# Performance work log

Measured on AMD Instinct MI355X. Metric: run time of the kernel, lower is better.

## Reference

```python
import jax, jax.numpy as jnp
import numpy as np

N_NODES = 50000
N_EDGES = 1600000
IN_CH = 256
LAT = 32
HID = 64
OUT_CH = 256
GAT_H = 32  # GAT hidden dims [32, 32], heads=1


def setup_inputs() -> dict:
    key = jax.random.key(0)
    ks = jax.random.split(key, 30)
    nrm = lambda k, shape, s=0.05: jax.random.normal(k, shape, dtype=jnp.float32) * s
    inp = {}
    inp["x"] = jax.random.normal(ks[0], (N_NODES, IN_CH), dtype=jnp.float32)
    inp["edge_index"] = jax.random.randint(ks[1], (2, N_EDGES), 0, N_NODES)
    # GAT layer 1: IN_CH -> 32 (heads=1), layer 2: 32 -> 32, final linear 32 -> LAT
    inp["W_g1"] = nrm(ks[2], (IN_CH, GAT_H)); inp["as_g1"] = nrm(ks[3], (GAT_H,)); inp["ad_g1"] = nrm(ks[4], (GAT_H,)); inp["b_g1"] = jnp.zeros((GAT_H,), jnp.float32)
    inp["W_g2"] = nrm(ks[5], (GAT_H, GAT_H)); inp["as_g2"] = nrm(ks[6], (GAT_H,)); inp["ad_g2"] = nrm(ks[7], (GAT_H,)); inp["b_g2"] = jnp.zeros((GAT_H,), jnp.float32)
    inp["W_gf"] = nrm(ks[8], (GAT_H, LAT)); inp["b_gf"] = jnp.zeros((LAT,), jnp.float32)
    inp["W_m1"] = nrm(ks[9], (IN_CH, HID)); inp["b_m1"] = jnp.zeros((HID,), jnp.float32); inp["g_m1"] = jnp.ones((HID,), jnp.float32); inp["be_m1"] = jnp.zeros((HID,), jnp.float32)
    inp["W_m2"] = nrm(ks[10], (HID, HID)); inp["b_m2"] = jnp.zeros((HID,), jnp.float32); inp["g_m2"] = jnp.ones((HID,), jnp.float32); inp["be_m2"] = jnp.zeros((HID,), jnp.float32)
    inp["W_m3"] = nrm(ks[11], (HID, LAT)); inp["b_m3"] = jnp.zeros((LAT,), jnp.float32); inp["g_m3"] = jnp.ones((LAT,), jnp.float32); inp["be_m3"] = jnp.zeros((LAT,), jnp.float32)
    # final linear LAT -> OUT_CH + ReLU
    inp["W_f"] = nrm(ks[12], (LAT, OUT_CH)); inp["b_f"] = jnp.zeros((OUT_CH,), jnp.float32)
    return inp


def _bn_relu(h, g, b):
    # BatchNorm1d in training mode: batch stats, biased variance, eps=1e-5
    m = jnp.mean(h, axis=0)
    v = jnp.var(h, axis=0)
    return jax.nn.relu((h - m) * jax.lax.rsqrt(v + 1e-5) * g + b)


def _gat(h_in, src, dst, W, a_s, a_d, b):
    # PyG GATConv (heads=1): edge (src j -> dst i), e = LeakyReLU(a_src.Wx_j + a_dst.Wx_i)
    N = h_in.shape[0]
    h = h_in @ W                                   # [N, F]
    e = jax.nn.leaky_relu((h @ a_s)[src] + (h @ a_d)[dst], 0.2)  # [E]
    m = jax.ops.segment_max(e, dst, num_segments=N)              # scatter-softmax over incoming edges
    ex = jnp.exp(e - m[dst])
    den = jax.ops.segment_sum(ex, dst, num_segments=N)
    alpha = ex / den[dst]
    out = jax.ops.segment_sum(alpha[:, None] * h[src], dst, num_segments=N)
    return out + b


def reference(x, edge_index, W_g1, as_g1, ad_g1, b_g1, W_g2, as_g2, ad_g2, b_g2, W_gf, b_gf, W_m1, b_m1, g_m1, be_m1, W_m2, b_m2, g_m2, be_m2, W_m3, b_m3, g_m3, be_m3, W_f, b_f):
    N = x.shape[0]
    loops = jnp.arange(N)
    src = jnp.concatenate([edge_index[0], loops])  # PyG add_self_loops=True
    dst = jnp.concatenate([edge_index[1], loops])
    r = _bn_relu(x @ W_m1 + b_m1, g_m1, be_m1)
    r = _bn_relu(r @ W_m2 + b_m2, g_m2, be_m2)
    r = _bn_relu(r @ W_m3 + b_m3, g_m3, be_m3)
    # GAT interpolation branch (dropout inactive in eval)
    h = jax.nn.relu(_gat(x, src, dst, W_g1, as_g1, ad_g1, b_g1))
    h = jax.nn.relu(_gat(h, src, dst, W_g2, as_g2, ad_g2, b_g2))
    h = h @ W_gf + b_gf
    # blend with alphas = 0.5 constant vector
    out = 0.5 * r + 0.5 * h
    return jax.nn.relu(out @ W_f + b_f)
```

## Files before the change

### kernel.cpp

```cpp
#include <hip/hip_runtime.h>

#define NNODES 50000
#define NEDGES 1600000
#define NBUCK 196
#define BIN_CH 4096
#define CNT_CH 4096

typedef __attribute__((ext_vector_type(4))) float f32x4;
typedef __attribute__((ext_vector_type(8))) short short8;

__device__ __forceinline__ float leaky02(float x) { return x > 0.f ? x : 0.2f * x; }

__device__ __forceinline__ int block_incl_scan(int v, int* sh) {
  int t = threadIdx.x;
  sh[t] = v;
  __syncthreads();
  for (int d = 1; d < 256; d <<= 1) {
    int u = (t >= d) ? sh[t - d] : 0;
    __syncthreads();
    sh[t] += u;
    __syncthreads();
  }
  return sh[t];
}

__global__ __launch_bounds__(256) void k_b0(const int* __restrict__ dst,
                                            int* __restrict__ gcnt, int E) {
  __shared__ int hist[256];
  int t = threadIdx.x;
  hist[t] = 0;
  __syncthreads();
  int base0 = blockIdx.x * CNT_CH;
#pragma unroll
  for (int r = 0; r < CNT_CH / 256; ++r) {
    int idx = base0 + r * 256 + t;
    if (idx < E) atomicAdd(&hist[dst[idx] >> 8], 1);
  }
  __syncthreads();
  if (t < NBUCK && hist[t]) atomicAdd(&gcnt[t], hist[t]);
}

__global__ __launch_bounds__(256) void k_b1(const int* __restrict__ gcnt,
                                            int* __restrict__ base,
                                            int* __restrict__ cursor) {
  __shared__ int sh[256];
  int t = threadIdx.x;
  int v = (t < NBUCK) ? gcnt[t] : 0;
  int incl = block_incl_scan(v, sh);
  if (t < NBUCK) {
    base[t] = incl - v;
    cursor[t] = incl - v;
  }
  if (t == 255) base[NBUCK] = NEDGES;
}

__global__ __launch_bounds__(256) void k_bin(const int* __restrict__ src,
                                             const int* __restrict__ dst,
                                             int* __restrict__ cursor,
                                             unsigned* __restrict__ binned, int E) {
  __shared__ int hist[256];
  __shared__ int cur[256];
  int t = threadIdx.x;
  int base0 = blockIdx.x * BIN_CH;
  unsigned pk[BIN_CH / 256];
  hist[t] = 0;
  __syncthreads();
#pragma unroll
  for (int r = 0; r < BIN_CH / 256; ++r) {
    int idx = base0 + r * 256 + t;
    if (idx < E) {
      unsigned p = ((unsigned)dst[idx] << 16) | (unsigned)src[idx];
      pk[r] = p;
      atomicAdd(&hist[p >> 24], 1);
    }
  }
  __syncthreads();
  if (t < NBUCK && hist[t]) cur[t] = atomicAdd(&cursor[t], hist[t]);
  __syncthreads();
#pragma unroll
  for (int r = 0; r < BIN_CH / 256; ++r) {
    int idx = base0 + r * 256 + t;
    if (idx < E) {
      unsigned p = pk[r];
      int pos = atomicAdd(&cur[p >> 24], 1);
      binned[pos] = p;
    }
  }
}

__global__ __launch_bounds__(256) void k_sort(const unsigned* __restrict__ binned,
                                              const int* __restrict__ base,
                                              int* __restrict__ deg,
                                              int* __restrict__ offs,
                                              int* __restrict__ csr) {
  __shared__ int hist[256];
  __shared__ int scanbuf[256];
  __shared__ int cur[256];
  int t = threadIdx.x;
  int b = blockIdx.x;
  int lo = base[b], hi = base[b + 1];
  int node0 = b << 8;
  hist[t] = 0;
  __syncthreads();
  for (int i = lo + t; i < hi; i += 256)
    atomicAdd(&hist[(binned[i] >> 16) & 255], 1);
  __syncthreads();
  int h = hist[t];
  int incl = block_incl_scan(h, scanbuf);
  int excl = incl - h;
  int node = node0 + t;
  if (node < NNODES) {
    deg[node] = h;
    offs[node] = lo + excl;
  }
  cur[t] = lo + excl;
  __syncthreads();
  for (int i = lo + t; i < hi; i += 256) {
    unsigned p = binned[i];
    int pos = atomicAdd(&cur[(p >> 16) & 255], 1);
    csr[pos] = (int)(p & 0xFFFFu);
  }
}

template <int K, int NC, int TN, int SPLIT, bool BN, bool STATS, int ROWS>
__global__ __launch_bounds__(256) void k_gemm(
    const float* __restrict__ A, const float* __restrict__ bn_sum,
    const float* __restrict__ bn_sq, const float* __restrict__ bn_gamma,
    const float* __restrict__ bn_beta, float invM,
    const float* __restrict__ B0, const float* __restrict__ B1,
    const float* __restrict__ bias0,
    float* __restrict__ out0, float* __restrict__ out1,
    float* __restrict__ gsum, float* __restrict__ gsq, int M) {
  constexpr int KC = 64;
  constexpr int RPT = ROWS / 16;
  __shared__ float As[ROWS * KC];
  __shared__ float Bs[KC * NC];
  __shared__ float scS[BN ? K : 4];
  __shared__ float shS[BN ? K : 4];
  const int tid = threadIdx.x;
  const int row0 = blockIdx.x * ROWS;
  const int cg = tid & 15;
  const int rowg = (tid >> 4) & 15;
  const int swz = (rowg & 3) << 2;

  if constexpr (BN) {
    if (tid < K) {
      float mean = bn_sum[tid] * invM;
      float var = bn_sq[tid] * invM - mean * mean;
      float rs = rsqrtf(var + 1e-5f);
      float sc = rs * bn_gamma[tid];
      scS[tid] = sc;
      shS[tid] = bn_beta[tid] - mean * sc;
    }
    __syncthreads();
  }

  float acc[RPT][TN];
#pragma unroll
  for (int r = 0; r < RPT; ++r)
#pragma unroll
    for (int j = 0; j < TN; ++j) acc[r][j] = 0.f;

  constexpr int KB = KC / 4;
  for (int k0 = 0; k0 < K; k0 += KC) {
#pragma unroll
    for (int it = 0; it < (ROWS * KB) / 256; ++it) {
      int idx = tid + it * 256;
      int row = idx / KB;
      int kb = idx % KB;
      float4 v = make_float4(0.f, 0.f, 0.f, 0.f);
      int grow = row0 + row;
      if (grow < M) {
        v = *reinterpret_cast<const float4*>(&A[(size_t)grow * K + k0 + kb * 4]);
        if constexpr (BN) {
          int kb4 = k0 + kb * 4;
          float4 sc = *reinterpret_cast<const float4*>(&scS[kb4]);
          float4 sf = *reinterpret_cast<const float4*>(&shS[kb4]);
          v.x = fmaxf(v.x * sc.x + sf.x, 0.f);
          v.y = fmaxf(v.y * sc.y + sf.y, 0.f);
          v.z = fmaxf(v.z * sc.z + sf.z, 0.f);
          v.w = fmaxf(v.w * sc.w + sf.w, 0.f);
        }
      }
      *reinterpret_cast<float4*>(&As[row * KC + ((kb ^ (row & 3)) * 4)]) = v;
    }
    {
      constexpr int KB0 = SPLIT / 4;
#pragma unroll
      for (int it = 0; it < (KC * KB0) / 256; ++it) {
        int idx = tid + it * 256;
        int kk = idx / KB0;
        int cb = idx % KB0;
        float4 v = *reinterpret_cast<const float4*>(&B0[(size_t)(k0 + kk) * SPLIT + cb * 4]);
        *reinterpret_cast<float4*>(&Bs[kk * NC + cb * 4]) = v;
      }
    }
    if constexpr (NC > SPLIT) {
      constexpr int W1 = NC - SPLIT;
      constexpr int KB1 = W1 / 4;
#pragma unroll
      for (int it = 0; it < (KC * KB1) / 256; ++it) {
        int idx = tid + it * 256;
        int kk = idx / KB1;
        int cb = idx % KB1;
        float4 v = *reinterpret_cast<const float4*>(&B1[(size_t)(k0 + kk) * W1 + cb * 4]);
        *reinterpret_cast<float4*>(&Bs[kk * NC + SPLIT + cb * 4]) = v;
      }
    }
    __syncthreads();
    for (int kk = 0; kk < KC; kk += 4) {
      float4 a[RPT];
#pragma unroll
      for (int r = 0; r < RPT; ++r)
        a[r] = *reinterpret_cast<const float4*>(&As[(rowg + 16 * r) * KC + (kk ^ swz)]);
      float b[4][TN];
#pragma unroll
      for (int i = 0; i < 4; ++i)
#pragma unroll
        for (int j = 0; j < TN; ++j) b[i][j] = Bs[(kk + i) * NC + cg * TN + j];
#pragma unroll
      for (int r = 0; r < RPT; ++r)
#pragma unroll
        for (int j = 0; j < TN; ++j) {
          acc[r][j] += a[r].x * b[0][j];
          acc[r][j] += a[r].y * b[1][j];
          acc[r][j] += a[r].z * b[2][j];
          acc[r][j] += a[r].w * b[3][j];
        }
    }
    __syncthreads();
  }
  float bias_r[TN];
#pragma unroll
  for (int j = 0; j < TN; ++j) {
    int c = cg * TN + j;
    bias_r[j] = (c < SPLIT) ? bias0[c] : 0.f;
  }
  float cs[TN], cq[TN];
#pragma unroll
  for (int j = 0; j < TN; ++j) { cs[j] = 0.f; cq[j] = 0.f; }
#pragma unroll
  for (int r = 0; r < RPT; ++r) {
    int grow = row0 + rowg + 16 * r;
    if (grow < M) {
#pragma unroll
      for (int j = 0; j < TN; ++j) {
        int c = cg * TN + j;
        if (c < SPLIT) {
          float v = acc[r][j] + bias_r[j];
          out0[(size_t)grow * SPLIT + c] = v;
          if (STATS) { cs[j] += v; cq[j] += v * v; }
        } else {
          out1[(size_t)grow * (NC - SPLIT) + (c - SPLIT)] = acc[r][j];
        }
      }
    }
  }
  if constexpr (STATS) {
#pragma unroll
    for (int j = 0; j < TN; ++j) {
      cs[j] += __shfl_xor(cs[j], 16);
      cs[j] += __shfl_xor(cs[j], 32);
      cq[j] += __shfl_xor(cq[j], 16);
      cq[j] += __shfl_xor(cq[j], 32);
    }
    float* red = Bs;
    int wave = tid >> 6;
    int lane = tid & 63;
    if (lane < 16) {
#pragma unroll
      for (int j = 0; j < TN; ++j) {
        int c = cg * TN + j;
        if (c < SPLIT) {
          red[wave * 2 * SPLIT + c] = cs[j];
          red[wave * 2 * SPLIT + SPLIT + c] = cq[j];
        }
      }
    }
    __syncthreads();
    if (tid < SPLIT) {
      float s = red[tid] + red[2 * SPLIT + tid] + red[4 * SPLIT + tid] + red[6 * SPLIT + tid];
      atomicAdd(&gsum[tid], s);
    } else if (tid < 2 * SPLIT) {
      int c = tid - SPLIT;
      float q = red[SPLIT + c] + red[3 * SPLIT + c] + red[5 * SPLIT + c] + red[7 * SPLIT + c];
      atomicAdd(&gsq[c], q);
    }
  }
}

__global__ __launch_bounds__(512) void k_bsplit(const float* __restrict__ Wm,
                                                const float* __restrict__ Wg,
                                                unsigned short* __restrict__ Bt) {
  int b = blockIdx.x;
  int cc = b / 6, cf = b % 6;
  int t = threadIdx.x;
  int lane = t >> 3, j = t & 7;
  int lg = lane >> 4, lc = lane & 15;
  int k = cc * 32 + lg * 8 + j;
  int col = cf * 16 + lc;
  float v = (col < 64) ? Wm[k * 64 + col] : Wg[k * 32 + (col - 64)];
  unsigned bb = __float_as_uint(v);
  unsigned h = bb & 0xffff0000u;
  float lo = v - __uint_as_float(h);
  Bt[(size_t)(b * 2 + 0) * 512 + t] = (unsigned short)(h >> 16);
  Bt[(size_t)(b * 2 + 1) * 512 + t] = (unsigned short)(__float_as_uint(lo) >> 16);
}

union U16 { uint4 u; short8 s; };
__device__ __forceinline__ short8 as_s8(uint4 u) { U16 t; t.u = u; return t.s; }

__device__ __forceinline__ void split2(float x0, float x1, unsigned& h, unsigned& l) {
  unsigned b0 = __float_as_uint(x0), b1 = __float_as_uint(x1);
  unsigned h0 = b0 & 0xffff0000u, h1 = b1 & 0xffff0000u;
  h = (h0 >> 16) | h1;
  float l0 = x0 - __uint_as_float(h0);
  float l1 = x1 - __uint_as_float(h1);
  l = (__float_as_uint(l0) >> 16) | (__float_as_uint(l1) & 0xffff0000u);
}

__device__ __forceinline__ void split8(const float4& a, const float4& b,
                                       short8& hi, short8& lo) {
  uint4 h, l;
  split2(a.x, a.y, h.x, l.x);
  split2(a.z, a.w, h.y, l.y);
  split2(b.x, b.y, h.z, l.z);
  split2(b.z, b.w, h.w, l.w);
  hi = as_s8(h);
  lo = as_s8(l);
}

__device__ __forceinline__ void gload16(const float* g, float* l) {
  __builtin_amdgcn_global_load_lds(
      (const __attribute__((address_space(1))) void*)g,
      (__attribute__((address_space(3))) void*)l, 16, 0, 0);
}

__global__ __launch_bounds__(256) void k_gemm1_mfma(
    const float* __restrict__ A, const unsigned short* __restrict__ Bt,
    const float* __restrict__ bias0,
    float* __restrict__ out0, float* __restrict__ out1,
    float* __restrict__ gsum, float* __restrict__ gsq, int M) {
  __shared__ float As[2][64 * 64];
  __shared__ float red[512];
  const int tid = threadIdx.x;
  const int wv = tid >> 6;
  const int lane = tid & 63;
  const int lg = lane >> 4;
  const int lc = lane & 15;
  const int wr = wv >> 1;
  const int wc = wv & 1;
  const int rowb = blockIdx.x * 64;

  const int sp = lane & 15;
  const int sr4 = lane >> 4;

  const int rl0 = wr * 32 + lc;
  const int rl1 = rl0 + 16;

  f32x4 acc[2][3];
#pragma unroll
  for (int rf = 0; rf < 2; ++rf)
#pragma unroll
    for (int j = 0; j < 3; ++j) acc[rf][j] = (f32x4){0.f, 0.f, 0.f, 0.f};

#pragma unroll
  for (int q = 0; q < 4; ++q) {
    int r = wv * 16 + q * 4 + sr4;
    int grow = rowb + r;
    grow = grow < M ? grow : M - 1;
    int s = sp ^ (r & 7);
    gload16(A + (size_t)grow * 256 + s * 4, &As[0][(wv * 16 + q * 4) * 64]);
  }
  __syncthreads();

#pragma unroll
  for (int c = 0; c < 4; ++c) {
    const int buf = c & 1;
    if (c < 3) {
#pragma unroll
      for (int q = 0; q < 4; ++q) {
        int r = wv * 16 + q * 4 + sr4;
        int grow = rowb + r;
        grow = grow < M ? grow : M - 1;
        int s = sp ^ (r & 7);
        gload16(A + (size_t)grow * 256 + (c + 1) * 64 + s * 4,
                &As[buf ^ 1][(wv * 16 + q * 4) * 64]);
      }
    }
    uint4 bhr[2][3], blr[2][3];
#pragma unroll
    for (int ks = 0; ks < 2; ++ks) {
      int cc = c * 2 + ks;
#pragma unroll
      for (int j = 0; j < 3; ++j) {
        const unsigned short* bp =
            Bt + (size_t)((cc * 6 + wc * 3 + j) * 2) * 512 + lane * 8;
        bhr[ks][j] = *reinterpret_cast<const uint4*>(bp);
        blr[ks][j] = *reinterpret_cast<const uint4*>(bp + 512);
      }
    }
#pragma unroll
    for (int ks = 0; ks < 2; ++ks) {
      const int s0 = ks * 8 + lg * 2;
      float4 a00 = *reinterpret_cast<const float4*>(
          &As[buf][rl0 * 64 + ((s0) ^ (rl0 & 7)) * 4]);
      float4 a01 = *reinterpret_cast<const float4*>(
          &As[buf][rl0 * 64 + ((s0 + 1) ^ (rl0 & 7)) * 4]);
      float4 a10 = *reinterpret_cast<const float4*>(
          &As[buf][rl1 * 64 + ((s0) ^ (rl1 & 7)) * 4]);
      float4 a11 = *reinterpret_cast<const float4*>(
          &As[buf][rl1 * 64 + ((s0 + 1) ^ (rl1 & 7)) * 4]);
      short8 ah0, al0, ah1, al1;
      split8(a00, a01, ah0, al0);
      split8(a10, a11, ah1, al1);
#pragma unroll
      for (int j = 0; j < 3; ++j) {
        short8 bh = as_s8(bhr[ks][j]), bl = as_s8(blr[ks][j]);
        acc[0][j] = __builtin_amdgcn_mfma_f32_16x16x32_bf16(ah0, bh, acc[0][j], 0, 0, 0);
        acc[0][j] = __builtin_amdgcn_mfma_f32_16x16x32_bf16(al0, bh, acc[0][j], 0, 0, 0);
        acc[0][j] = __builtin_amdgcn_mfma_f32_16x16x32_bf16(ah0, bl, acc[0][j], 0, 0, 0);
        acc[1][j] = __builtin_amdgcn_mfma_f32_16x16x32_bf16(ah1, bh, acc[1][j], 0, 0, 0);
        acc[1][j] = __builtin_amdgcn_mfma_f32_16x16x32_bf16(al1, bh, acc[1][j], 0, 0, 0);
        acc[1][j] = __builtin_amdgcn_mfma_f32_16x16x32_bf16(ah1, bl, acc[1][j], 0, 0, 0);
      }
    }
    __syncthreads();
  }

  red[tid] = 0.f;
  red[tid + 256] = 0.f;
  __syncthreads();

  float bias_r[3];
#pragma unroll
  for (int j = 0; j < 3; ++j) {
    int gcf = wc * 3 + j;
    bias_r[j] = (gcf < 4) ? bias0[gcf * 16 + lc] : 0.f;
  }
  float cs[3] = {0.f, 0.f, 0.f}, cq[3] = {0.f, 0.f, 0.f};
#pragma unroll
  for (int rf = 0; rf < 2; ++rf) {
    int rbase = rowb + wr * 32 + rf * 16 + lg * 4;
#pragma unroll
    for (int i = 0; i < 4; ++i) {
      int row = rbase + i;
      if (row < M) {
#pragma unroll
        for (int j = 0; j < 3; ++j) {
          int gcf = wc * 3 + j;
          if (gcf < 4) {
            float v = acc[rf][j][i] + bias_r[j];
            out0[(size_t)row * 64 + gcf * 16 + lc] = v;
            cs[j] += v;
            cq[j] += v * v;
          } else {
            out1[(size_t)row * 32 + (gcf - 4) * 16 + lc] = acc[rf][j][i];
          }
        }
      }
    }
  }
#pragma unroll
  for (int j = 0; j < 3; ++j) {
    cs[j] += __shfl_xor(cs[j], 16);
    cs[j] += __shfl_xor(cs[j], 32);
    cq[j] += __shfl_xor(cq[j], 16);
    cq[j] += __shfl_xor(cq[j], 32);
  }
  if (lg == 0) {
#pragma unroll
    for (int j = 0; j < 3; ++j) {
      int gcf = wc * 3 + j;
      if (gcf < 4) {
        red[wv * 128 + gcf * 16 + lc] = cs[j];
        red[wv * 128 + 64 + gcf * 16 + lc] = cq[j];
      }
    }
  }
  __syncthreads();
  if (tid < 64) {
    atomicAdd(&gsum[tid], red[tid] + red[128 + tid] + red[256 + tid] + red[384 + tid]);
  } else if (tid < 128) {
    int cc2 = tid - 64;
    atomicAdd(&gsq[cc2], red[64 + cc2] + red[192 + cc2] + red[320 + cc2] + red[448 + cc2]);
  }
}

__global__ __launch_bounds__(256) void k_sdot(const float* __restrict__ g,
                                              const float* __restrict__ as_,
                                              const float* __restrict__ ad_,
                                              float* __restrict__ sv,
                                              float* __restrict__ dv, int N) {
  int lane = threadIdx.x & 31;
  int row = blockIdx.x * 8 + (threadIdx.x >> 5);
  if (row >= N) return;
  float v = g[(size_t)row * 32 + lane];
  float a = v * as_[lane];
  float b = v * ad_[lane];
#pragma unroll
  for (int w = 16; w >= 1; w >>= 1) {
    a += __shfl_xor(a, w);
    b += __shfl_xor(b, w);
  }
  if (lane == 0) {
    sv[row] = a;
    dv[row] = b;
  }
}

__global__ __launch_bounds__(256) void k_gat_agg(
    const float* __restrict__ h, const float* __restrict__ sv,
    const float* __restrict__ dv, const int* __restrict__ offs,
    const int* __restrict__ deg, const int* __restrict__ csr,
    const float* __restrict__ bias, float* __restrict__ out, int N) {
  int lane = threadIdx.x & 31;
  int node = blockIdx.x * 8 + (threadIdx.x >> 5);
  if (node >= N) return;
  int start = offs[node];
  int cnt = deg[node];
  float di = dv[node];
  float ex0 = __expf(leaky02(sv[node] + di));
  float den = ex0;
  float acc = ex0 * h[(size_t)node * 32 + lane];
  int k = 0;
  for (; k + 8 <= cnt; k += 8) {
    int j0 = csr[start + k + 0], j1 = csr[start + k + 1];
    int j2 = csr[start + k + 2], j3 = csr[start + k + 3];
    int j4 = csr[start + k + 4], j5 = csr[start + k + 5];
    int j6 = csr[start + k + 6], j7 = csr[start + k + 7];
    float s0 = sv[j0], s1 = sv[j1], s2 = sv[j2], s3 = sv[j3];
    float s4 = sv[j4], s5 = sv[j5], s6 = sv[j6], s7 = sv[j7];
    float h0 = h[(size_t)j0 * 32 + lane], h1 = h[(size_t)j1 * 32 + lane];
    float h2 = h[(size_t)j2 * 32 + lane], h3 = h[(size_t)j3 * 32 + lane];
    float h4 = h[(size_t)j4 * 32 + lane], h5 = h[(size_t)j5 * 32 + lane];
    float h6 = h[(size_t)j6 * 32 + lane], h7 = h[(size_t)j7 * 32 + lane];
    float e0 = __expf(leaky02(s0 + di)), e1 = __expf(leaky02(s1 + di));
    float e2 = __expf(leaky02(s2 + di)), e3 = __expf(leaky02(s3 + di));
    float e4 = __expf(leaky02(s4 + di)), e5 = __expf(leaky02(s5 + di));
    float e6 = __expf(leaky02(s6 + di)), e7 = __expf(leaky02(s7 + di));
    den += ((e0 + e1) + (e2 + e3)) + ((e4 + e5) + (e6 + e7));
    acc += e0 * h0 + e1 * h1 + e2 * h2 + e3 * h3;
    acc += e4 * h4 + e5 * h5 + e6 * h6 + e7 * h7;
  }
  for (; k < cnt; ++k) {
    int j = csr[start + k];
    float ex = __expf(leaky02(sv[j] + di));
    den += ex;
    acc += ex * h[(size_t)j * 32 + lane];
  }
  out[(size_t)node * 32 + lane] = fmaxf(acc / den + bias[lane], 0.f);
}

__global__ __launch_bounds__(256) void k_small_gemm_sd(
    const float* __restrict__ hin, const float* __restrict__ W,
    const float* __restrict__ as_, const float* __restrict__ ad_,
    float* __restrict__ gout, float* __restrict__ sv, float* __restrict__ dv,
    int N) {
  __shared__ float Ws[32][32];
  {
    int t = threadIdx.x;
#pragma unroll
    for (int r = 0; r < 4; ++r) {
      int idx = t + r * 256;
      Ws[idx >> 5][idx & 31] = W[idx];
    }
  }
  __syncthreads();
  int lane = threadIdx.x & 31;
  int row = blockIdx.x * 8 + (threadIdx.x >> 5);
  if (row >= N) return;
  float hv = hin[(size_t)row * 32 + lane];
  float acc = 0.f;
#pragma unroll
  for (int k = 0; k < 32; ++k) acc += __shfl(hv, k, 32) * Ws[k][lane];
  gout[(size_t)row * 32 + lane] = acc;
  float a = acc * as_[lane];
  float b = acc * ad_[lane];
#pragma unroll
  for (int w = 16; w >= 1; w >>= 1) {
    a += __shfl_xor(a, w);
    b += __shfl_xor(b, w);
  }
  if (lane == 0) {
    sv[row] = a;
    dv[row] = b;
  }
}

__global__ __launch_bounds__(256) void k_final2(
    const float* __restrict__ mlp3, const float* __restrict__ sum3,
    const float* __restrict__ sq3, const float* __restrict__ g3,
    const float* __restrict__ be3, float invM, const float* __restrict__ h2,
    const float* __restrict__ Wgf, const float* __restrict__ bgf,
    const float* __restrict__ Wf, const float* __restrict__ bf,
    float* __restrict__ out, int N) {
  __shared__ float WfS[32 * 256];
  __shared__ float Bl[64][36];
  __shared__ float WgfS[32][33];
  __shared__ float colS[3][32];
  const int t = threadIdx.x;
  const int row0 = blockIdx.x * 64;

  {
    const float4* src = reinterpret_cast<const float4*>(Wf);
    float4* dst = reinterpret_cast<float4*>(WfS);
#pragma unroll
    for (int r = 0; r < 8; ++r) dst[t + r * 256] = src[t + r * 256];
  }
#pragma unroll
  for (int r = 0; r < 4; ++r) {
    int idx = t + r * 256;
    WgfS[idx >> 5][idx & 31] = Wgf[idx];
  }
  if (t < 32) {
    float mean = sum3[t] * invM;
    float var = sq3[t] * invM - mean * mean;
    float rs = rsqrtf(var + 1e-5f);
    float sc = rs * g3[t];
    colS[0][t] = sc;
    colS[1][t] = be3[t] - mean * sc;
    colS[2][t] = bgf[t];
  }
#pragma unroll
  for (int r = 0; r < 2; ++r) {
    int idx = t + r * 256;
    int row = idx >> 3;
    int k4 = idx & 7;
    int grow = row0 + row;
    float4 v = make_float4(0.f, 0.f, 0.f, 0.f);
    if (grow < N) v = *reinterpret_cast<const float4*>(&h2[(size_t)grow * 32 + k4 * 4]);
    *reinterpret_cast<float4*>(&Bl[row][k4 * 4]) = v;
  }
  __syncthreads();

  const int col = t & 31;
  const int rb = t >> 5;
  float w[32];
#pragma unroll
  for (int k = 0; k < 32; ++k) w[k] = WgfS[k][col];
  float bl[8];
#pragma unroll
  for (int r = 0; r < 8; ++r) {
    int row = rb + 8 * r;
    float a = colS[2][col];
#pragma unroll
    for (int k4 = 0; k4 < 8; ++k4) {
      float4 hv = *reinterpret_cast<const float4*>(&Bl[row][k4 * 4]);
      a += hv.x * w[k4 * 4 + 0] + hv.y * w[k4 * 4 + 1] +
           hv.z * w[k4 * 4 + 2] + hv.w * w[k4 * 4 + 3];
    }
    int grow = row0 + row;
    float pre = (grow < N) ? mlp3[(size_t)grow * 32 + col] : 0.f;
    float rv = fmaxf(pre * colS[0][col] + colS[1][col], 0.f);
    bl[r] = 0.5f * rv + 0.5f * a;
  }
  __syncthreads();
#pragma unroll
  for (int r = 0; r < 8; ++r) Bl[rb + 8 * r][col] = bl[r];
  __syncthreads();

  const int cg = t & 31;
  const int rowg = t >> 5;
  const float4* Wf4 = reinterpret_cast<const float4*>(WfS);
  float4 acc0[8], acc1[8];
#pragma unroll
  for (int r = 0; r < 8; ++r) {
    acc0[r] = make_float4(0.f, 0.f, 0.f, 0.f);
    acc1[r] = make_float4(0.f, 0.f, 0.f, 0.f);
  }
  for (int k = 0; k < 32; k += 4) {
    float4 a[8];
#pragma unroll
    for (int r = 0; r < 8; ++r)
      a[r] = *reinterpret_cast<const float4*>(&Bl[rowg + 8 * r][k]);
    float4 b0[4], b1[4];
#pragma unroll
    for (int i = 0; i < 4; ++i) {
      b0[i] = Wf4[(k + i) * 64 + cg];
      b1[i] = Wf4[(k + i) * 64 + cg + 32];
    }
#pragma unroll
    for (int r = 0; r < 8; ++r) {
      float av[4] = {a[r].x, a[r].y, a[r].z, a[r].w};
#pragma unroll
      for (int i = 0; i < 4; ++i) {
        acc0[r].x += av[i] * b0[i].x;
        acc0[r].y += av[i] * b0[i].y;
        acc0[r].z += av[i] * b0[i].z;
        acc0[r].w += av[i] * b0[i].w;
        acc1[r].x += av[i] * b1[i].x;
        acc1[r].y += av[i] * b1[i].y;
        acc1[r].z += av[i] * b1[i].z;
        acc1[r].w += av[i] * b1[i].w;
      }
    }
  }
  float4 bfA = reinterpret_cast<const float4*>(bf)[cg];
  float4 bfB = reinterpret_cast<const float4*>(bf)[cg + 32];
  float4* out4 = reinterpret_cast<float4*>(out);
#pragma unroll
  for (int r = 0; r < 8; ++r) {
    int grow = row0 + rowg + 8 * r;
    if (grow < N) {
      float4 o0 = acc0[r], o1 = acc1[r];
      o0.x = fmaxf(o0.x + bfA.x, 0.f); o0.y = fmaxf(o0.y + bfA.y, 0.f);
      o0.z = fmaxf(o0.z + bfA.z, 0.f); o0.w = fmaxf(o0.w + bfA.w, 0.f);
      o1.x = fmaxf(o1.x + bfB.x, 0.f); o1.y = fmaxf(o1.y + bfB.y, 0.f);
      o1.z = fmaxf(o1.z + bfB.z, 0.f); o1.w = fmaxf(o1.w + bfB.w, 0.f);
      out4[(size_t)grow * 64 + cg] = o0;
      out4[(size_t)grow * 64 + cg + 32] = o1;
    }
  }
}

extern "C" void kernel_launch(void* const* d_in, const int* in_sizes, int n_in,
                              void* d_out, int out_size, void* d_ws, size_t ws_size,
                              hipStream_t stream) {
  const float* x = (const float*)d_in[0];
  const int* edge = (const int*)d_in[1];
  const float* W_g1 = (const float*)d_in[2];
  const float* as_g1 = (const float*)d_in[3];
  const float* ad_g1 = (const float*)d_in[4];
  const float* b_g1 = (const float*)d_in[5];
  const float* W_g2 = (const float*)d_in[6];
  const float* as_g2 = (const float*)d_in[7];
  const float* ad_g2 = (const float*)d_in[8];
  const float* b_g2 = (const float*)d_in[9];
  const float* W_gf = (const float*)d_in[10];
  const float* b_gf = (const float*)d_in[11];
  const float* W_m1 = (const float*)d_in[12];
  const float* b_m1 = (const float*)d_in[13];
  const float* g_m1 = (const float*)d_in[14];
  const float* be_m1 = (const float*)d_in[15];
  const float* W_m2 = (const float*)d_in[16];
  const float* b_m2 = (const float*)d_in[17];
  const float* g_m2 = (const float*)d_in[18];
  const float* be_m2 = (const float*)d_in[19];
  const float* W_m3 = (const float*)d_in[20];
  const float* b_m3 = (const float*)d_in[21];
  const float* g_m3 = (const float*)d_in[22];
  const float* be_m3 = (const float*)d_in[23];
  const float* W_f = (const float*)d_in[24];
  const float* b_f = (const float*)d_in[25];
  float* out = (float*)d_out;

  const int N = NNODES, E = NEDGES;
  const float invM = 1.f / N;
  const int* esrc = edge;
  const int* edst = edge + E;

  float* ws = (float*)d_ws;
  float* g1 = ws;
  float* mlp1 = g1 + (size_t)N * 32;
  float* mlp2 = mlp1 + (size_t)N * 64;
  float* mlp3 = mlp2 + (size_t)N * 64;
  float* h1 = mlp3 + (size_t)N * 32;
  float* g2 = h1 + (size_t)N * 32;
  float* h2 = g2 + (size_t)N * 32;
  float* s1 = h2 + (size_t)N * 32;
  float* d1 = s1 + N;
  float* s2 = d1 + N;
  float* d2 = s2 + N;
  float* stats = d2 + N;
  float* sum1 = stats, *sq1 = stats + 64;
  float* sum2 = stats + 128, *sq2 = stats + 192;
  float* sum3 = stats + 256, *sq3 = stats + 288;
  int* ip = (int*)(stats + 384);
  int* gcnt = ip;
  int* base = gcnt + 256;
  int* cursor = base + 256;
  int* deg = cursor + 256;
  int* offs = deg + N;
  int* csr = offs + N;
  unsigned* binned = (unsigned*)mlp2;
  unsigned short* Bt = (unsigned short*)((char*)mlp2 + (size_t)E * 4);

  hipMemsetAsync(gcnt, 0, 256 * sizeof(int), stream);
  hipMemsetAsync(stats, 0, 384 * sizeof(float), stream);

  k_bsplit<<<48, 512, 0, stream>>>(W_m1, W_g1, Bt);

  k_b0<<<(E + CNT_CH - 1) / CNT_CH, 256, 0, stream>>>(edst, gcnt, E);
  k_b1<<<1, 256, 0, stream>>>(gcnt, base, cursor);
  k_bin<<<(E + BIN_CH - 1) / BIN_CH, 256, 0, stream>>>(esrc, edst, cursor, binned, E);
  k_sort<<<NBUCK, 256, 0, stream>>>(binned, base, deg, offs, csr);

  const int GB64 = (N + 63) / 64;
  const int GB128 = (N + 127) / 128;

  k_gemm1_mfma<<<GB64, 256, 0, stream>>>(x, Bt, b_m1, mlp1, g1, sum1, sq1, N);
  k_sdot<<<(N + 7) / 8, 256, 0, stream>>>(g1, as_g1, ad_g1, s1, d1, N);
  k_gat_agg<<<(N + 7) / 8, 256, 0, stream>>>(g1, s1, d1, offs, deg, csr, b_g1, h1, N);

  k_gemm<64, 64, 4, 64, true, true, 128><<<GB128, 256, 0, stream>>>(
      mlp1, sum1, sq1, g_m1, be_m1, invM, W_m2, nullptr, b_m2,
      mlp2, nullptr, sum2, sq2, N);

  k_small_gemm_sd<<<(N + 7) / 8, 256, 0, stream>>>(h1, W_g2, as_g2, ad_g2, g2, s2, d2, N);
  k_gat_agg<<<(N + 7) / 8, 256, 0, stream>>>(g2, s2, d2, offs, deg, csr, b_g2, h2, N);

  k_gemm<64, 32, 2, 32, true, true, 128><<<GB128, 256, 0, stream>>>(
      mlp2, sum2, sq2, g_m2, be_m2, invM, W_m3, nullptr, b_m3,
      mlp3, nullptr, sum3, sq3, N);

  k_final2<<<(N + 63) / 64, 256, 0, stream>>>(mlp3, sum3, sq3, g_m3, be_m3, invM,
                                              h2, W_gf, b_gf, W_f, b_f, out, N);
}
```

Baseline: 399.2 us.

## Stage split-bf16 weights in LDS and enlarge gemm1 tile to 128 rows

The first fused GEMM (x @ [W_m1|W_g1]) now copies the whole pre-split bf16 hi/lo weight matrix into shared memory once per block, using global_load_lds. Before, every wave re-read it from global memory on each K step. Blocks grow to 512 threads covering 128 rows, and the K loop moves to 32-wide chunks over 8 iterations with a narrower double-buffered A tile. This aims to cut redundant global weight traffic and amortize it over more rows. In exchange it uses roughly 130KB of LDS per block, which limits occupancy, and adds more barrier-synchronised iterations.

```diff
diff --git a/kernel.cpp b/kernel.cpp
--- a/kernel.cpp
+++ b/kernel.cpp
@@ -330,19 +330,20 @@
   lo = as_s8(l);
 }
 
-__device__ __forceinline__ void gload16(const float* g, float* l) {
+__device__ __forceinline__ void gload16(const void* g, void* l) {
   __builtin_amdgcn_global_load_lds(
       (const __attribute__((address_space(1))) void*)g,
       (__attribute__((address_space(3))) void*)l, 16, 0, 0);
 }
 
-__global__ __launch_bounds__(256) void k_gemm1_mfma(
+__global__ __launch_bounds__(512, 2) void k_gemm1_mfma(
     const float* __restrict__ A, const unsigned short* __restrict__ Bt,
     const float* __restrict__ bias0,
     float* __restrict__ out0, float* __restrict__ out1,
     float* __restrict__ gsum, float* __restrict__ gsq, int M) {
-  __shared__ float As[2][64 * 64];
-  __shared__ float red[512];
+  __shared__ unsigned short BsS[49152];
+  __shared__ float As[2][128 * 32];
+  __shared__ float red[1024];
   const int tid = threadIdx.x;
   const int wv = tid >> 6;
   const int lane = tid & 63;
@@ -350,10 +351,10 @@
   const int lc = lane & 15;
   const int wr = wv >> 1;
   const int wc = wv & 1;
-  const int rowb = blockIdx.x * 64;
-
-  const int sp = lane & 15;
-  const int sr4 = lane >> 4;
+  const int rowb = blockIdx.x * 128;
+
+  const int srow = lane >> 3;
+  const int sfetch = (lane & 7) ^ srow;
 
   const int rl0 = wr * 32 + lc;
   const int rl1 = rl0 + 16;
@@ -364,72 +365,70 @@
 #pragma unroll
     for (int j = 0; j < 3; ++j) acc[rf][j] = (f32x4){0.f, 0.f, 0.f, 0.f};
 
-#pragma unroll
-  for (int q = 0; q < 4; ++q) {
-    int r = wv * 16 + q * 4 + sr4;
-    int grow = rowb + r;
+  {
+    const char* bsrc = (const char*)Bt;
+    char* bdst = (char*)BsS;
+#pragma unroll
+    for (int i = 0; i < 12; ++i) {
+      int off = i * 8192 + wv * 1024;
+      gload16(bsrc + off + lane * 16, bdst + off);
+    }
+  }
+#pragma unroll
+  for (int q = 0; q < 2; ++q) {
+    int lrow = wv * 16 + q * 8 + srow;
+    int grow = rowb + lrow;
     grow = grow < M ? grow : M - 1;
-    int s = sp ^ (r & 7);
-    gload16(A + (size_t)grow * 256 + s * 4, &As[0][(wv * 16 + q * 4) * 64]);
-  }
-  __syncthreads();
-
-#pragma unroll
-  for (int c = 0; c < 4; ++c) {
+    gload16(A + (size_t)grow * 256 + sfetch * 4, &As[0][(wv * 16 + q * 8) * 32]);
+  }
+  __syncthreads();
+
+#pragma unroll
+  for (int c = 0; c < 8; ++c) {
     const int buf = c & 1;
-    if (c < 3) {
-#pragma unroll
-      for (int q = 0; q < 4; ++q) {
-        int r = wv * 16 + q * 4 + sr4;
-        int grow = rowb + r;
+    if (c < 7) {
+#pragma unroll
+      for (int q = 0; q < 2; ++q) {
+        int lrow = wv * 16 + q * 8 + srow;
+        int grow = rowb + lrow;
         grow = grow < M ? grow : M - 1;
-        int s = sp ^ (r & 7);
-        gload16(A + (size_t)grow * 256 + (c + 1) * 64 + s * 4,
-                &As[buf ^ 1][(wv * 16 + q * 4) * 64]);
+        gload16(A + (size_t)grow * 256 + (c + 1) * 32 + sfetch * 4,
+                &As[buf ^ 1][(wv * 16 + q * 8) * 32]);
       }
     }
-    uint4 bhr[2][3], blr[2][3];
-#pragma unroll
-    for (int ks = 0; ks < 2; ++ks) {
-      int cc = c * 2 + ks;
-#pragma unroll
-      for (int j = 0; j < 3; ++j) {
-        const unsigned short* bp =
-            Bt + (size_t)((cc * 6 + wc * 3 + j) * 2) * 512 + lane * 8;
-        bhr[ks][j] = *reinterpret_cast<const uint4*>(bp);
-        blr[ks][j] = *reinterpret_cast<const uint4*>(bp + 512);
-      }
-    }
-#pragma unroll
-    for (int ks = 0; ks < 2; ++ks) {
-      const int s0 = ks * 8 + lg * 2;
-      float4 a00 = *reinterpret_cast<const float4*>(
-          &As[buf][rl0 * 64 + ((s0) ^ (rl0 & 7)) * 4]);
-      float4 a01 = *reinterpret_cast<const float4*>(
-          &As[buf][rl0 * 64 + ((s0 + 1) ^ (rl0 & 7)) * 4]);
-      float4 a10 = *reinterpret_cast<const float4*>(
-          &As[buf][rl1 * 64 + ((s0) ^ (rl1 & 7)) * 4]);
-      float4 a11 = *reinterpret_cast<const float4*>(
-          &As[buf][rl1 * 64 + ((s0 + 1) ^ (rl1 & 7)) * 4]);
-      short8 ah0, al0, ah1, al1;
-      split8(a00, a01, ah0, al0);
-      split8(a10, a11, ah1, al1);
-#pragma unroll
-      for (int j = 0; j < 3; ++j) {
-        short8 bh = as_s8(bhr[ks][j]), bl = as_s8(blr[ks][j]);
-        acc[0][j] = __builtin_amdgcn_mfma_f32_16x16x32_bf16(ah0, bh, acc[0][j], 0, 0, 0);
-        acc[0][j] = __builtin_amdgcn_mfma_f32_16x16x32_bf16(al0, bh, acc[0][j], 0, 0, 0);
-        acc[0][j] = __builtin_amdgcn_mfma_f32_16x16x32_bf16(ah0, bl, acc[0][j], 0, 0, 0);
-        acc[1][j] = __builtin_amdgcn_mfma_f32_16x16x32_bf16(ah1, bh, acc[1][j], 0, 0, 0);
-        acc[1][j] = __builtin_amdgcn_mfma_f32_16x16x32_bf16(al1, bh, acc[1][j], 0, 0, 0);
-        acc[1][j] = __builtin_amdgcn_mfma_f32_16x16x32_bf16(ah1, bl, acc[1][j], 0, 0, 0);
-      }
+    uint4 bhr[3], blr[3];
+#pragma unroll
+    for (int j = 0; j < 3; ++j) {
+      const unsigned short* bp = &BsS[((c * 6 + wc * 3 + j) * 2) * 512 + lane * 8];
+      bhr[j] = *reinterpret_cast<const uint4*>(bp);
+      blr[j] = *reinterpret_cast<const uint4*>(bp + 512);
+    }
+    float4 a00 = *reinterpret_cast<const float4*>(
+        &As[buf][rl0 * 32 + ((2 * lg) ^ (rl0 & 7)) * 4]);
+    float4 a01 = *reinterpret_cast<const float4*>(
+        &As[buf][rl0 * 32 + ((2 * lg + 1) ^ (rl0 & 7)) * 4]);
+    float4 a10 = *reinterpret_cast<const float4*>(
+        &As[buf][rl1 * 32 + ((2 * lg) ^ (rl1 & 7)) * 4]);
+    float4 a11 = *reinterpret_cast<const float4*>(
+        &As[buf][rl1 * 32 + ((2 * lg + 1) ^ (rl1 & 7)) * 4]);
+    short8 ah0, al0, ah1, al1;
+    split8(a00, a01, ah0, al0);
+    split8(a10, a11, ah1, al1);
+#pragma unroll
+    for (int j = 0; j < 3; ++j) {
+      short8 bh = as_s8(bhr[j]), bl = as_s8(blr[j]);
+      acc[0][j] = __builtin_amdgcn_mfma_f32_16x16x32_bf16(ah0, bh, acc[0][j], 0, 0, 0);
+      acc[0][j] = __builtin_amdgcn_mfma_f32_16x16x32_bf16(al0, bh, acc[0][j], 0, 0, 0);
+      acc[0][j] = __builtin_amdgcn_mfma_f32_16x16x32_bf16(ah0, bl, acc[0][j], 0, 0, 0);
+      acc[1][j] = __builtin_amdgcn_mfma_f32_16x16x32_bf16(ah1, bh, acc[1][j], 0, 0, 0);
+      acc[1][j] = __builtin_amdgcn_mfma_f32_16x16x32_bf16(al1, bh, acc[1][j], 0, 0, 0);
+      acc[1][j] = __builtin_amdgcn_mfma_f32_16x16x32_bf16(ah1, bl, acc[1][j], 0, 0, 0);
     }
     __syncthreads();
   }
 
   red[tid] = 0.f;
-  red[tid + 256] = 0.f;
+  red[tid + 512] = 0.f;
   __syncthreads();
 
   float bias_r[3];
@@ -480,10 +479,16 @@
   }
   __syncthreads();
   if (tid < 64) {
-    atomicAdd(&gsum[tid], red[tid] + red[128 + tid] + red[256 + tid] + red[384 + tid]);
+    float s = 0.f;
+#pragma unroll
+    for (int w = 0; w < 8; ++w) s += red[w * 128 + tid];
+    atomicAdd(&gsum[tid], s);
   } else if (tid < 128) {
     int cc2 = tid - 64;
-    atomicAdd(&gsq[cc2], red[64 + cc2] + red[192 + cc2] + red[320 + cc2] + red[448 + cc2]);
+    float q = 0.f;
+#pragma unroll
+    for (int w = 0; w < 8; ++w) q += red[w * 128 + 64 + cc2];
+    atomicAdd(&gsq[cc2], q);
   }
 }
 
@@ -789,7 +794,7 @@
   const int GB64 = (N + 63) / 64;
   const int GB128 = (N + 127) / 128;
 
-  k_gemm1_mfma<<<GB64, 256, 0, stream>>>(x, Bt, b_m1, mlp1, g1, sum1, sq1, N);
+  k_gemm1_mfma<<<GB128, 512, 0, stream>>>(x, Bt, b_m1, mlp1, g1, sum1, sq1, N);
   k_sdot<<<(N + 7) / 8, 256, 0, stream>>>(g1, as_g1, ad_g1, s1, d1, N);
   k_gat_agg<<<(N + 7) / 8, 256, 0, stream>>>(g1, s1, d1, offs, deg, csr, b_g1, h1, N);
 
```

Measured after the change: 396.7 us. Within noise of the previous version (-0.6%).
